# Performance work log

Hardware: AMD Instinct MI355X
Metric: run time of the kernel (lower is better)

## Reference

```python
import jax, jax.numpy as jnp
import numpy as np

# COCO-17 body parts (padded to max length with -1)
_PARTS = [[0,1,2,3,4],[5,6,11,12],[5,7,9],[6,8,10],[11,13,15],[12,14,16]]
_P = len(_PARTS)
_L = max(len(p) for p in _PARTS)
_IDX_NP = np.full((_P, _L), -1, dtype=np.int32)
for _p, _ix in enumerate(_PARTS):
    _IDX_NP[_p, :len(_ix)] = _ix
SAFE_IDX = jnp.asarray(np.clip(_IDX_NP, 0, None))   # (P,L)
VALID = jnp.asarray(_IDX_NP >= 0)                   # (P,L)
NUM_HEADS = 4
LN_EPS = 1e-5


def setup_inputs() -> dict:
    key = jax.random.key(0)
    ks = jax.random.split(key, 8)
    B, T, J, D = 32, 512, 17, 128
    s = 1.0 / np.sqrt(D)
    return {
        "h_joint": jax.random.normal(ks[0], (B, T, J, D), jnp.float32),
        "mask_joint": jax.random.uniform(ks[1], (B, T, J, 1), jnp.float32),
        "W_proj": jax.random.normal(ks[2], (D, D), jnp.float32) * s,
        "b_proj": jnp.zeros((D,), jnp.float32),
        "W_in": jax.random.normal(ks[3], (3 * D, D), jnp.float32) * s,
        "b_in": jnp.zeros((3 * D,), jnp.float32),
        "W_out": jax.random.normal(ks[4], (D, D), jnp.float32) * s,
        "b_out": jnp.zeros((D,), jnp.float32),
        "ln_g": jnp.ones((D,), jnp.float32),
        "ln_b": jnp.zeros((D,), jnp.float32),
    }


def reference(h_joint, mask_joint, W_proj, b_proj, W_in, b_in, W_out, b_out, ln_g, ln_b):
    B, T, J, D = h_joint.shape
    P, L = SAFE_IDX.shape
    H = NUM_HEADS
    dh = D // H

    # 1) gather joints per part + 2) mask-aware mean pool -> part tokens (B,T,P,D)
    m = mask_joint[..., 0] > 0.05                      # (B,T,J) bool
    hg = jnp.take(h_joint, SAFE_IDX, axis=2)           # (B,T,P,L,D)
    mg = jnp.take(m, SAFE_IDX, axis=2) & VALID         # (B,T,P,L)
    mf = mg.astype(h_joint.dtype)
    denom = jnp.clip(jnp.sum(mf, axis=3), 1e-6, None)  # (B,T,P)
    tok = jnp.einsum('btpld,btpl->btpd', hg, mf) / denom[..., None]

    tok = tok @ W_proj.T + b_proj                      # proj_in

    # 3) MHA across parts per frame (eval mode: dropout off)
    BT = B * T
    q = tok.reshape(BT, P, D)
    qkv = q @ W_in.T + b_in                            # (BT,P,3D)
    qh, kh, vh = (a.reshape(BT, P, H, dh).transpose(0, 2, 1, 3)
                  for a in jnp.split(qkv, 3, axis=-1))  # each (BT,H,P,dh)
    scores = jnp.einsum('bhqd,bhkd->bhqk', qh, kh) / np.sqrt(dh)
    w = jax.nn.softmax(scores, axis=-1)                # (BT,H,P,P)
    o = jnp.einsum('bhqk,bhkd->bhqd', w, vh)
    o = o.transpose(0, 2, 1, 3).reshape(BT, P, D) @ W_out.T + b_out

    # 4) residual + LayerNorm
    y = q + o
    mu = jnp.mean(y, axis=-1, keepdims=True)
    var = jnp.mean(jnp.square(y - mu), axis=-1, keepdims=True)
    y = (y - mu) * jax.lax.rsqrt(var + LN_EPS) * ln_g + ln_b

    part_out = y.reshape(B, T, P, D)
    attn_weights = jnp.mean(w, axis=1)                 # avg heads -> (BT,P,P)
    part_importance = jnp.mean(attn_weights, axis=1).reshape(B, T, P)
    return part_out, part_importance
```

## Files before the change

kernel.cpp:

```cpp
#include <hip/hip_runtime.h>
#include <hip/hip_bf16.h>

typedef __hip_bfloat16 bf16;
typedef __attribute__((ext_vector_type(8))) short short8v;
typedef __attribute__((ext_vector_type(4))) float f32x4;

#define NJ   17
#define ND   128
#define NP   6
#define NH   4
#define NBT  16384
#define NG   4
#define NTOK (NG*NP)
#define NTHR 512
#define GRID (NBT/NG)
#define TSTR 136
#define YSTR 132

#define WS_WP 0
#define WS_WC 16384
#define WS_WO 65536
#define WS_BC 163840
#define WS_MB 165376

#define OFF_POOL 0
#define OFF_TOKP 6528
#define OFF_Q    13056
#define OFF_K    19584
#define OFF_V    26112
#define OFF_Y    19584
#define OFF_PROB 32640
#define OFF_MU   34944
#define OFF_INV  35040
#define ARENA_SZ 35136

__device__ __forceinline__ float bf2f(unsigned short u) {
    return __uint_as_float(((unsigned)u) << 16);
}
__device__ __forceinline__ unsigned pk2(float x, float y) {
    bf16 bx = __float2bfloat16(x), by = __float2bfloat16(y);
    unsigned short ux = *reinterpret_cast<unsigned short*>(&bx);
    unsigned short uy = *reinterpret_cast<unsigned short*>(&by);
    return ((unsigned)uy << 16) | ux;
}
__device__ __forceinline__ f32x4 MFMA(short8v a, short8v b, f32x4 c) {
    return __builtin_amdgcn_mfma_f32_16x16x32_bf16(a, b, c, 0, 0, 0);
}
__device__ __forceinline__ short8v ldB(const bf16* __restrict__ W, int nt, int ks, int lane) {
    return *reinterpret_cast<const short8v*>(W + (nt*16 + (lane & 15))*ND + ks*32 + ((lane >> 4) << 3));
}
__device__ __forceinline__ short8v ldsA(const bf16* __restrict__ s, int mt, int ks, int lane) {
    int row = mt*16 + (lane & 15);
    if (row >= NTOK) row = NTOK - 1;
    return *reinterpret_cast<const short8v*>(s + row*TSTR + ks*32 + ((lane >> 4) << 3));
}
__device__ __forceinline__ void bsync() {
    asm volatile("s_waitcnt lgkmcnt(0)" ::: "memory");
    __builtin_amdgcn_s_barrier();
    asm volatile("" ::: "memory");
}
#define WFENCE() do { \
    asm volatile("s_waitcnt lgkmcnt(0)" ::: "memory"); \
    __builtin_amdgcn_sched_barrier(0); \
} while (0)

extern "C" __global__ __launch_bounds__(128)
void prep(const float* __restrict__ Wp, const float* __restrict__ Wi,
          const float* __restrict__ Wo, const float* __restrict__ bp,
          const float* __restrict__ bi, const float* __restrict__ mask,
          bf16* __restrict__ wgt, float* __restrict__ bc,
          unsigned* __restrict__ mbuf) {
    const int b = blockIdx.x, t = threadIdx.x;
    if (b < 384) {
        __shared__ float s_wi[128];
        __shared__ float s_red[128];
        s_wi[t] = Wi[b*128 + t];
        __syncthreads();
        float acc = 0.f;
        #pragma unroll 8
        for (int m = 0; m < 128; ++m)
            acc = fmaf(s_wi[m], Wp[m*128 + t], acc);
        wgt[WS_WC + b*128 + t] = __float2bfloat16(acc);
        s_red[t] = s_wi[t] * bp[t];
        __syncthreads();
        #pragma unroll
        for (int s = 64; s > 0; s >>= 1) {
            if (t < s) s_red[t] += s_red[t+s];
            __syncthreads();
        }
        if (t == 0) bc[b] = s_red[0] + bi[b];
    } else {
        int gid = (b - 384)*128 + t;
        if (gid < 16384) wgt[WS_WP + gid] = __float2bfloat16(Wp[gid]);
        else             wgt[WS_WO + (gid - 16384)] = __float2bfloat16(Wo[gid - 16384]);
        if (gid < 16384) {
            const float* m = mask + (long)gid*NJ;
            unsigned bb = 0;
            #pragma unroll
            for (int j = 0; j < NJ; ++j)
                bb |= (m[j] > 0.05f) ? (1u << j) : 0u;
            mbuf[gid] = bb;
        }
    }
}

__device__ __forceinline__ void st24(bf16* __restrict__ dst, const f32x4 &a0,
                                     const f32x4 &a1, float bv, int col, int lhi) {
    #pragma unroll
    for (int j = 0; j < 4; ++j) {
        int r0 = lhi*4 + j;
        dst[r0*TSTR + col] = __float2bfloat16(a0[j] + bv);
        int r1 = 16 + lhi*4 + j;
        if (r1 < NTOK) dst[r1*TSTR + col] = __float2bfloat16(a1[j] + bv);
    }
}

extern "C" __global__ __launch_bounds__(NTHR, 6)
void bpa_fused(const float* __restrict__ h_joint,
               const bf16* __restrict__ wgt, const float* __restrict__ bc,
               const unsigned* __restrict__ mbuf,
               const float* __restrict__ b_proj, const float* __restrict__ b_out,
               const float* __restrict__ ln_g,  const float* __restrict__ ln_b,
               float* __restrict__ out)
{
    __shared__ __align__(16) unsigned char s_arena[ARENA_SZ];
    bf16*  s_pool  = reinterpret_cast<bf16*>(s_arena + OFF_POOL);
    bf16*  s_tokp  = reinterpret_cast<bf16*>(s_arena + OFF_TOKP);
    bf16*  s_q     = reinterpret_cast<bf16*>(s_arena + OFF_Q);
    bf16*  s_k     = reinterpret_cast<bf16*>(s_arena + OFF_K);
    bf16*  s_v     = reinterpret_cast<bf16*>(s_arena + OFF_V);
    float* s_y     = reinterpret_cast<float*>(s_arena + OFF_Y);
    float* s_probs = reinterpret_cast<float*>(s_arena + OFF_PROB);
    float* s_mu    = reinterpret_cast<float*>(s_arena + OFF_MU);
    float* s_inv   = reinterpret_cast<float*>(s_arena + OFF_INV);

    const int tid  = threadIdx.x;
    const int lane = tid & 63;
    const int w    = tid >> 6;
    const int l15  = lane & 15;
    const int lhi  = lane >> 4;
    const long frame0 = (long)blockIdx.x * NG;

    {
        const int f = tid >> 7;
        const int d = tid & (ND-1);
        const float* hcol = h_joint + (frame0 + f)*(long)(NJ*ND) + d;
        float hv[NJ];
        #pragma unroll
        for (int j = 0; j < NJ; ++j) hv[j] = hcol[j*ND];
        unsigned mb = mbuf[frame0 + f];
        #pragma unroll
        for (int j = 0; j < NJ; ++j)
            hv[j] = (mb >> j & 1) ? hv[j] : 0.f;
        float acc[NP];
        acc[0] = ((hv[0]+hv[1]) + (hv[2]+hv[3])) + hv[4];
        acc[1] = (hv[5]+hv[6]) + (hv[11]+hv[12]);
        acc[2] = hv[5]+hv[7]+hv[9];
        acc[3] = hv[6]+hv[8]+hv[10];
        acc[4] = hv[11]+hv[13]+hv[15];
        acc[5] = hv[12]+hv[14]+hv[16];
        const unsigned pm[NP] = {0x1Fu, 0x1860u, 0x2A0u, 0x540u, 0xA800u, 0x15000u};
        #pragma unroll
        for (int p = 0; p < NP; ++p) {
            float cnt = (float)__popc(mb & pm[p]);
            s_pool[(f*NP+p)*TSTR + d] = __float2bfloat16(acc[p] / fmaxf(cnt, 1e-6f));
        }
    }
    bsync();

    {
        const int col = w*16 + l15;
        short8v bA[4], bB[4];
        #pragma unroll
        for (int ks = 0; ks < 4; ++ks) bA[ks] = ldB(wgt + WS_WP, w, ks, lane);
        #pragma unroll
        for (int ks = 0; ks < 4; ++ks) bB[ks] = ldB(wgt + WS_WC, w, ks, lane);
        {
            f32x4 a0 = (f32x4)(0.f), a1 = (f32x4)(0.f);
            #pragma unroll
            for (int ks = 0; ks < 4; ++ks) {
                a0 = MFMA(ldsA(s_pool, 0, ks, lane), bA[ks], a0);
                a1 = MFMA(ldsA(s_pool, 1, ks, lane), bA[ks], a1);
            }
            st24(s_tokp, a0, a1, b_proj[col], col, lhi);
        }
        #pragma unroll
        for (int ks = 0; ks < 4; ++ks) bA[ks] = ldB(wgt + WS_WC, 8 + w, ks, lane);
        {
            f32x4 a0 = (f32x4)(0.f), a1 = (f32x4)(0.f);
            #pragma unroll
            for (int ks = 0; ks < 4; ++ks) {
                a0 = MFMA(ldsA(s_pool, 0, ks, lane), bB[ks], a0);
                a1 = MFMA(ldsA(s_pool, 1, ks, lane), bB[ks], a1);
            }
            st24(s_q, a0, a1, bc[w*16 + l15], col, lhi);
        }
        #pragma unroll
        for (int ks = 0; ks < 4; ++ks) bB[ks] = ldB(wgt + WS_WC, 16 + w, ks, lane);
        {
            f32x4 a0 = (f32x4)(0.f), a1 = (f32x4)(0.f);
            #pragma unroll
            for (int ks = 0; ks < 4; ++ks) {
                a0 = MFMA(ldsA(s_pool, 0, ks, lane), bA[ks], a0);
                a1 = MFMA(ldsA(s_pool, 1, ks, lane), bA[ks], a1);
            }
            st24(s_k, a0, a1, bc[(8+w)*16 + l15], col, lhi);
        }
        {
            f32x4 a0 = (f32x4)(0.f), a1 = (f32x4)(0.f);
            #pragma unroll
            for (int ks = 0; ks < 4; ++ks) {
                a0 = MFMA(ldsA(s_pool, 0, ks, lane), bB[ks], a0);
                a1 = MFMA(ldsA(s_pool, 1, ks, lane), bB[ks], a1);
            }
            st24(s_v, a0, a1, bc[(16+w)*16 + l15], col, lhi);
        }
    }
    bsync();

    short8v bo[4];
    #pragma unroll
    for (int ks = 0; ks < 4; ++ks) bo[ks] = ldB(wgt + WS_WO, w, ks, lane);

    if (w < NG) {
        const int fq = w;
        float* s_pr = s_probs + fq*(NH*NP*NP);
        const int arow = (fq*NP + (l15 > 5 ? 5 : l15))*TSTR + (lhi << 3);
        float imp = 0.f;
        #pragma unroll
        for (int h = 0; h < NH; ++h) {
            short8v qa = *reinterpret_cast<const short8v*>(s_q + arow + h*32);
            short8v kb = *reinterpret_cast<const short8v*>(s_k + arow + h*32);
            f32x4 c = MFMA(qa, kb, (f32x4)(0.f));
            #pragma unroll
            for (int j = 0; j < 4; ++j) {
                int q = lhi*4 + j;
                float sc  = c[j] * 0.17677669529663688f;
                float scm = (l15 < NP) ? sc : -1e30f;
                scm = fmaxf(scm, __shfl_xor(scm, 1));
                scm = fmaxf(scm, __shfl_xor(scm, 2));
                scm = fmaxf(scm, __shfl_xor(scm, 4));
                scm = fmaxf(scm, __shfl_xor(scm, 8));
                float e = (l15 < NP) ? __expf(sc - scm) : 0.f;
                float den = e;
                den += __shfl_xor(den, 1);
                den += __shfl_xor(den, 2);
                den += __shfl_xor(den, 4);
                den += __shfl_xor(den, 8);
                float p = e / den;
                if (q < NP) {
                    imp += p;
                    if (l15 < NP) s_pr[(h*NP + q)*NP + l15] = p;
                }
            }
        }
        imp += __shfl_xor(imp, 16);
        imp += __shfl_xor(imp, 32);
        if (lane < NP)
            out[(long)NBT*NP*ND + (frame0 + fq)*NP + lane] = imp * (1.f/24.f);
        WFENCE();
        {
            const int c0 = lane*2;
            const int h  = lane >> 4;
            const float* pr = s_pr + h*NP*NP;
            float vx[NP], vy[NP];
            #pragma unroll
            for (int pk = 0; pk < NP; ++pk) {
                unsigned vv = *reinterpret_cast<const unsigned*>(&s_v[(fq*NP+pk)*TSTR + c0]);
                vx[pk] = bf2f((unsigned short)(vv & 0xFFFF));
                vy[pk] = bf2f((unsigned short)(vv >> 16));
            }
            #pragma unroll
            for (int qi = 0; qi < NP; ++qi) {
                const float* pq = pr + qi*NP;
                float ox = pq[0]*vx[0]+pq[1]*vx[1]+pq[2]*vx[2]
                         + pq[3]*vx[3]+pq[4]*vx[4]+pq[5]*vx[5];
                float oy = pq[0]*vy[0]+pq[1]*vy[1]+pq[2]*vy[2]
                         + pq[3]*vy[3]+pq[4]*vy[4]+pq[5]*vy[5];
                *reinterpret_cast<unsigned*>(&s_q[(fq*NP+qi)*TSTR + c0]) = pk2(ox, oy);
            }
        }
    }
    bsync();

    {
        f32x4 a0 = (f32x4)(0.f), a1 = (f32x4)(0.f);
        #pragma unroll
        for (int ks = 0; ks < 4; ++ks) {
            a0 = MFMA(ldsA(s_q, 0, ks, lane), bo[ks], a0);
            a1 = MFMA(ldsA(s_q, 1, ks, lane), bo[ks], a1);
        }
        int col = w*16 + l15;
        float bv = b_out[col];
        #pragma unroll
        for (int j = 0; j < 4; ++j) {
            int r0 = lhi*4 + j;
            float res0 = bf2f(*reinterpret_cast<const unsigned short*>(&s_tokp[r0*TSTR + col]));
            s_y[r0*YSTR + col] = a0[j] + bv + res0;
            int r1 = 16 + lhi*4 + j;
            if (r1 < NTOK) {
                float res1 = bf2f(*reinterpret_cast<const unsigned short*>(&s_tokp[r1*TSTR + col]));
                s_y[r1*YSTR + col] = a1[j] + bv + res1;
            }
        }
    }
    bsync();

    if (tid < NTOK*4) {
        int token = tid >> 2, sub = tid & 3;
        const float* row = s_y + token*YSTR + sub*32;
        float s = 0.f, s2 = 0.f;
        #pragma unroll
        for (int j = 0; j < 32; j += 4) {
            float4 v = *reinterpret_cast<const float4*>(row + j);
            s  += v.x + v.y + v.z + v.w;
            s2 += v.x*v.x + v.y*v.y + v.z*v.z + v.w*v.w;
        }
        s  += __shfl_xor(s, 1);  s  += __shfl_xor(s, 2);
        s2 += __shfl_xor(s2, 1); s2 += __shfl_xor(s2, 2);
        float mean = s * (1.f/128.f);
        float var  = s2 * (1.f/128.f) - mean*mean;
        if (sub == 0) {
            s_mu[token]  = mean;
            s_inv[token] = rsqrtf(var + 1e-5f);
        }
    }
    bsync();

    #pragma unroll
    for (int i = 0; i < 2; ++i) {
        int idx4 = i*NTHR + tid;
        if (idx4 < NTOK*(ND/4)) {
            int token = idx4 >> 5;
            int dj = (idx4 & 31) << 2;
            float mean = s_mu[token], inv = s_inv[token];
            float4 v = *reinterpret_cast<const float4*>(s_y + token*YSTR + dj);
            float4 g = *reinterpret_cast<const float4*>(ln_g + dj);
            float4 b = *reinterpret_cast<const float4*>(ln_b + dj);
            float4 r;
            r.x = (v.x-mean)*inv*g.x + b.x;
            r.y = (v.y-mean)*inv*g.y + b.y;
            r.z = (v.z-mean)*inv*g.z + b.z;
            r.w = (v.w-mean)*inv*g.w + b.w;
            *reinterpret_cast<float4*>(out + (frame0*NP + token)*(long)ND + dj) = r;
        }
    }
}

extern "C" void kernel_launch(void* const* d_in, const int* in_sizes, int n_in,
                              void* d_out, int out_size, void* d_ws, size_t ws_size,
                              hipStream_t stream) {
    const float* h_joint = (const float*)d_in[0];
    const float* mask    = (const float*)d_in[1];
    const float* W_proj  = (const float*)d_in[2];
    const float* b_proj  = (const float*)d_in[3];
    const float* W_in    = (const float*)d_in[4];
    const float* b_in    = (const float*)d_in[5];
    const float* W_out   = (const float*)d_in[6];
    const float* b_out   = (const float*)d_in[7];
    const float* ln_g    = (const float*)d_in[8];
    const float* ln_b    = (const float*)d_in[9];
    float* out = (float*)d_out;
    bf16*     wgt  = (bf16*)d_ws;
    float*    bc   = (float*)((char*)d_ws + WS_BC);
    unsigned* mbuf = (unsigned*)((char*)d_ws + WS_MB);

    hipLaunchKernelGGL(prep, dim3(640), dim3(128), 0, stream,
                       W_proj, W_in, W_out, b_proj, b_in, mask, wgt, bc, mbuf);
    hipLaunchKernelGGL(bpa_fused, dim3(GRID), dim3(NTHR), 0, stream,
                       h_joint, wgt, bc, mbuf, b_proj, b_out, ln_g, ln_b, out);
}
```

Measured before the change: 119.8 us.

## Keep projected tokens in registers, fuse LayerNorm per wave, raise occupancy

The proj_in result now stays in MFMA accumulator registers (tk0/tk1) for the residual instead of being written to LDS as bf16 and read back. This removes the s_tokp buffer and shrinks the shared arena, and the launch bound goes from 6 to 8 blocks per CU. LayerNorm now runs one wave per three tokens with full-wave shuffle reductions, which drops a barrier and the mu/inv LDS staging. The W_out load moves later to ease register pressure. The trade is more live registers across the attention phase, which may conflict with the higher occupancy target, and the residual now uses fp32 instead of bf16-rounded values.

```diff
diff --git a/kernel.cpp b/kernel.cpp
--- a/kernel.cpp
+++ b/kernel.cpp
@@ -24,15 +24,12 @@
 #define WS_MB 165376
 
 #define OFF_POOL 0
-#define OFF_TOKP 6528
-#define OFF_Q    13056
-#define OFF_K    19584
-#define OFF_V    26112
-#define OFF_Y    19584
-#define OFF_PROB 32640
-#define OFF_MU   34944
-#define OFF_INV  35040
-#define ARENA_SZ 35136
+#define OFF_Q    6528
+#define OFF_K    13056
+#define OFF_V    19584
+#define OFF_Y    13056
+#define OFF_PROB 26112
+#define ARENA_SZ 28416
 
 __device__ __forceinline__ float bf2f(unsigned short u) {
     return __uint_as_float(((unsigned)u) << 16);
@@ -115,7 +112,7 @@
     }
 }
 
-extern "C" __global__ __launch_bounds__(NTHR, 6)
+extern "C" __global__ __launch_bounds__(NTHR, 8)
 void bpa_fused(const float* __restrict__ h_joint,
                const bf16* __restrict__ wgt, const float* __restrict__ bc,
                const unsigned* __restrict__ mbuf,
@@ -125,14 +122,11 @@
 {
     __shared__ __align__(16) unsigned char s_arena[ARENA_SZ];
     bf16*  s_pool  = reinterpret_cast<bf16*>(s_arena + OFF_POOL);
-    bf16*  s_tokp  = reinterpret_cast<bf16*>(s_arena + OFF_TOKP);
     bf16*  s_q     = reinterpret_cast<bf16*>(s_arena + OFF_Q);
     bf16*  s_k     = reinterpret_cast<bf16*>(s_arena + OFF_K);
     bf16*  s_v     = reinterpret_cast<bf16*>(s_arena + OFF_V);
     float* s_y     = reinterpret_cast<float*>(s_arena + OFF_Y);
     float* s_probs = reinterpret_cast<float*>(s_arena + OFF_PROB);
-    float* s_mu    = reinterpret_cast<float*>(s_arena + OFF_MU);
-    float* s_inv   = reinterpret_cast<float*>(s_arena + OFF_INV);
 
     const int tid  = threadIdx.x;
     const int lane = tid & 63;
@@ -168,13 +162,32 @@
     }
     bsync();
 
+    f32x4 tk0 = (f32x4)(0.f), tk1 = (f32x4)(0.f);
     {
+        short8v bA[4], bB[4];
+        #pragma unroll
+        for (int ks = 0; ks < 4; ++ks) bA[ks] = ldB(wgt + WS_WP, w, ks, lane);
+        #pragma unroll
+        for (int ks = 0; ks < 4; ++ks) bB[ks] = ldB(wgt + WS_WC, w, ks, lane);
+        #pragma unroll
+        for (int ks = 0; ks < 4; ++ks) {
+            tk0 = MFMA(ldsA(s_pool, 0, ks, lane), bA[ks], tk0);
+            tk1 = MFMA(ldsA(s_pool, 1, ks, lane), bA[ks], tk1);
+        }
+        #pragma unroll
+        for (int ks = 0; ks < 4; ++ks) bA[ks] = ldB(wgt + WS_WC, 8 + w, ks, lane);
         const int col = w*16 + l15;
-        short8v bA[4], bB[4];
-        #pragma unroll
-        for (int ks = 0; ks < 4; ++ks) bA[ks] = ldB(wgt + WS_WP, w, ks, lane);
-        #pragma unroll
-        for (int ks = 0; ks < 4; ++ks) bB[ks] = ldB(wgt + WS_WC, w, ks, lane);
+        {
+            f32x4 a0 = (f32x4)(0.f), a1 = (f32x4)(0.f);
+            #pragma unroll
+            for (int ks = 0; ks < 4; ++ks) {
+                a0 = MFMA(ldsA(s_pool, 0, ks, lane), bB[ks], a0);
+                a1 = MFMA(ldsA(s_pool, 1, ks, lane), bB[ks], a1);
+            }
+            st24(s_q, a0, a1, bc[w*16 + l15], col, lhi);
+        }
+        #pragma unroll
+        for (int ks = 0; ks < 4; ++ks) bB[ks] = ldB(wgt + WS_WC, 16 + w, ks, lane);
         {
             f32x4 a0 = (f32x4)(0.f), a1 = (f32x4)(0.f);
             #pragma unroll
@@ -182,10 +195,8 @@
                 a0 = MFMA(ldsA(s_pool, 0, ks, lane), bA[ks], a0);
                 a1 = MFMA(ldsA(s_pool, 1, ks, lane), bA[ks], a1);
             }
-            st24(s_tokp, a0, a1, b_proj[col], col, lhi);
-        }
-        #pragma unroll
-        for (int ks = 0; ks < 4; ++ks) bA[ks] = ldB(wgt + WS_WC, 8 + w, ks, lane);
+            st24(s_k, a0, a1, bc[(8+w)*16 + l15], col, lhi);
+        }
         {
             f32x4 a0 = (f32x4)(0.f), a1 = (f32x4)(0.f);
             #pragma unroll
@@ -193,34 +204,10 @@
                 a0 = MFMA(ldsA(s_pool, 0, ks, lane), bB[ks], a0);
                 a1 = MFMA(ldsA(s_pool, 1, ks, lane), bB[ks], a1);
             }
-            st24(s_q, a0, a1, bc[w*16 + l15], col, lhi);
-        }
-        #pragma unroll
-        for (int ks = 0; ks < 4; ++ks) bB[ks] = ldB(wgt + WS_WC, 16 + w, ks, lane);
-        {
-            f32x4 a0 = (f32x4)(0.f), a1 = (f32x4)(0.f);
-            #pragma unroll
-            for (int ks = 0; ks < 4; ++ks) {
-                a0 = MFMA(ldsA(s_pool, 0, ks, lane), bA[ks], a0);
-                a1 = MFMA(ldsA(s_pool, 1, ks, lane), bA[ks], a1);
-            }
-            st24(s_k, a0, a1, bc[(8+w)*16 + l15], col, lhi);
-        }
-        {
-            f32x4 a0 = (f32x4)(0.f), a1 = (f32x4)(0.f);
-            #pragma unroll
-            for (int ks = 0; ks < 4; ++ks) {
-                a0 = MFMA(ldsA(s_pool, 0, ks, lane), bB[ks], a0);
-                a1 = MFMA(ldsA(s_pool, 1, ks, lane), bB[ks], a1);
-            }
             st24(s_v, a0, a1, bc[(16+w)*16 + l15], col, lhi);
         }
     }
     bsync();
-
-    short8v bo[4];
-    #pragma unroll
-    for (int ks = 0; ks < 4; ++ks) bo[ks] = ldB(wgt + WS_WO, w, ks, lane);
 
     if (w < NG) {
         const int fq = w;
@@ -284,6 +271,9 @@
     bsync();
 
     {
+        short8v bo[4];
+        #pragma unroll
+        for (int ks = 0; ks < 4; ++ks) bo[ks] = ldB(wgt + WS_WO, w, ks, lane);
         f32x4 a0 = (f32x4)(0.f), a1 = (f32x4)(0.f);
         #pragma unroll
         for (int ks = 0; ks < 4; ++ks) {
@@ -291,58 +281,39 @@
             a1 = MFMA(ldsA(s_q, 1, ks, lane), bo[ks], a1);
         }
         int col = w*16 + l15;
-        float bv = b_out[col];
+        float bb = b_proj[col] + b_out[col];
         #pragma unroll
         for (int j = 0; j < 4; ++j) {
             int r0 = lhi*4 + j;
-            float res0 = bf2f(*reinterpret_cast<const unsigned short*>(&s_tokp[r0*TSTR + col]));
-            s_y[r0*YSTR + col] = a0[j] + bv + res0;
+            s_y[r0*YSTR + col] = a0[j] + tk0[j] + bb;
             int r1 = 16 + lhi*4 + j;
-            if (r1 < NTOK) {
-                float res1 = bf2f(*reinterpret_cast<const unsigned short*>(&s_tokp[r1*TSTR + col]));
-                s_y[r1*YSTR + col] = a1[j] + bv + res1;
-            }
+            if (r1 < NTOK) s_y[r1*YSTR + col] = a1[j] + tk1[j] + bb;
         }
     }
     bsync();
 
-    if (tid < NTOK*4) {
-        int token = tid >> 2, sub = tid & 3;
-        const float* row = s_y + token*YSTR + sub*32;
-        float s = 0.f, s2 = 0.f;
-        #pragma unroll
-        for (int j = 0; j < 32; j += 4) {
-            float4 v = *reinterpret_cast<const float4*>(row + j);
-            s  += v.x + v.y + v.z + v.w;
-            s2 += v.x*v.x + v.y*v.y + v.z*v.z + v.w*v.w;
-        }
-        s  += __shfl_xor(s, 1);  s  += __shfl_xor(s, 2);
-        s2 += __shfl_xor(s2, 1); s2 += __shfl_xor(s2, 2);
-        float mean = s * (1.f/128.f);
-        float var  = s2 * (1.f/128.f) - mean*mean;
-        if (sub == 0) {
-            s_mu[token]  = mean;
-            s_inv[token] = rsqrtf(var + 1e-5f);
-        }
-    }
-    bsync();
-
-    #pragma unroll
-    for (int i = 0; i < 2; ++i) {
-        int idx4 = i*NTHR + tid;
-        if (idx4 < NTOK*(ND/4)) {
-            int token = idx4 >> 5;
-            int dj = (idx4 & 31) << 2;
-            float mean = s_mu[token], inv = s_inv[token];
-            float4 v = *reinterpret_cast<const float4*>(s_y + token*YSTR + dj);
-            float4 g = *reinterpret_cast<const float4*>(ln_g + dj);
-            float4 b = *reinterpret_cast<const float4*>(ln_b + dj);
-            float4 r;
-            r.x = (v.x-mean)*inv*g.x + b.x;
-            r.y = (v.y-mean)*inv*g.y + b.y;
-            r.z = (v.z-mean)*inv*g.z + b.z;
-            r.w = (v.w-mean)*inv*g.w + b.w;
-            *reinterpret_cast<float4*>(out + (frame0*NP + token)*(long)ND + dj) = r;
+    {
+        const int c0 = lane*2;
+        float2 g2 = *reinterpret_cast<const float2*>(ln_g + c0);
+        float2 b2 = *reinterpret_cast<const float2*>(ln_b + c0);
+        #pragma unroll
+        for (int ti = 0; ti < 3; ++ti) {
+            int token = w*3 + ti;
+            float2 v = *reinterpret_cast<const float2*>(s_y + token*YSTR + c0);
+            float s  = v.x + v.y;
+            float s2 = v.x*v.x + v.y*v.y;
+            s  += __shfl_xor(s, 1);  s  += __shfl_xor(s, 2);
+            s  += __shfl_xor(s, 4);  s  += __shfl_xor(s, 8);
+            s  += __shfl_xor(s, 16); s  += __shfl_xor(s, 32);
+            s2 += __shfl_xor(s2, 1); s2 += __shfl_xor(s2, 2);
+            s2 += __shfl_xor(s2, 4); s2 += __shfl_xor(s2, 8);
+            s2 += __shfl_xor(s2, 16); s2 += __shfl_xor(s2, 32);
+            float mean = s * (1.f/128.f);
+            float rinv = rsqrtf(s2 * (1.f/128.f) - mean*mean + 1e-5f);
+            float2 r;
+            r.x = (v.x - mean)*rinv*g2.x + b2.x;
+            r.y = (v.y - mean)*rinv*g2.y + b2.y;
+            *reinterpret_cast<float2*>(out + (frame0*NP + token)*(long)ND + c0) = r;
         }
     }
 }
```

Measured after the change: 159.3 us. +33.0%, slower.
